# Kernel optimization log

Measured on AMD Instinct MI355X. Metric: run time of the kernel, lower is better.

The kernel has to match this reference:

```python
import jax, jax.numpy as jnp
import numpy as np

HEADS = 8
DIM_HEAD = 64
DOWN = 2

def setup_inputs() -> dict:
    key = jax.random.key(0)
    ks = jax.random.split(key, 6)
    shp = (1, 128, 16, 32, 32)
    inner = HEADS * DIM_HEAD  # 512
    return {
        "x": jax.random.normal(ks[0], shp, dtype=jnp.float32),
        "context": jax.random.normal(ks[1], shp, dtype=jnp.float32),
        "Wq": jax.random.normal(ks[2], (inner, 128), dtype=jnp.float32) * 0.02,
        "Wk": jax.random.normal(ks[3], (inner, 128), dtype=jnp.float32) * 0.02,
        "Wv": jax.random.normal(ks[4], (inner, 128), dtype=jnp.float32) * 0.02,
        "Wo": jax.random.normal(ks[5], (128, inner), dtype=jnp.float32) * 0.02,
    }

def _avg_pool3d(c, f):
    b, ch, d, h, w = c.shape
    return c.reshape(b, ch, d // f, f, h // f, f, w // f, f).mean(axis=(3, 5, 7))

def reference(x, context, Wq, Wk, Wv, Wo):
    b, c, d1, h1, w1 = x.shape
    n = d1 * h1 * w1
    scale = DIM_HEAD ** -0.5
    xf = x.reshape(b, c, n)  # [b, c, N]
    # 1x1x1 conv == channel matmul
    q = jnp.einsum('oc,bcn->bon', Wq, xf).reshape(b, HEADS, DIM_HEAD, n)
    q = jnp.swapaxes(q, -2, -1)  # [b, h, N, dh]
    ctx = _avg_pool3d(context, DOWN)
    _, _, d2, h2, w2 = ctx.shape
    m = d2 * h2 * w2
    cf = ctx.reshape(b, c, m)
    k = jnp.einsum('oc,bcm->bom', Wk, cf).reshape(b, HEADS, DIM_HEAD, m)  # [b,h,dh,M]
    v = jnp.einsum('oc,bcm->bom', Wv, cf).reshape(b, HEADS, DIM_HEAD, m)
    v = jnp.swapaxes(v, -2, -1)  # [b, h, M, dh]
    scores = jnp.einsum('bhnd,bhdm->bhnm', q, k) * scale  # [b,h,N,M]
    attn = jax.nn.softmax(scores, axis=-1)
    out = jnp.einsum('bhnm,bhmd->bhnd', attn, v)  # [b,h,N,dh]
    out = jnp.swapaxes(out, -2, -1).reshape(b, HEADS * DIM_HEAD, n)  # [b,inner,N]
    y = jnp.einsum('oc,bcn->bon', Wo, out)
    return y.reshape(b, -1, d1, h1, w1)
```

## Files before the change

### kernel.cpp

```cpp
#include <hip/hip_runtime.h>

#define N_TOK 16384
#define M_TOK 2048
#define NHEADS 8
#define DH 64
#define CIN 128
#define INNER 512

typedef __attribute__((ext_vector_type(8))) short bf16x8;
typedef __attribute__((ext_vector_type(16))) float f32x16;
typedef __attribute__((ext_vector_type(4))) unsigned int u32x4;
typedef __attribute__((ext_vector_type(2))) unsigned int u32x2;

__device__ __forceinline__ unsigned short f2bf(float f) {
    unsigned u = __float_as_uint(f);
    u += 0x7fff + ((u >> 16) & 1);
    return (unsigned short)(u >> 16);
}

__device__ __forceinline__ unsigned cvtpk(float lo, float hi) {
    unsigned r;
    asm("v_cvt_pk_bf16_f32 %0, %1, %2" : "=v"(r) : "v"(lo), "v"(hi));
    return r;
}

__device__ __forceinline__ bf16x8 mk_bf16x8(unsigned a, unsigned b, unsigned c, unsigned d) {
    union { u32x4 w; bf16x8 h; } u;
    u.w = (u32x4){a, b, c, d};
    return u.h;
}

__device__ __forceinline__ void gload16(const void* g, void* l) {
    __builtin_amdgcn_global_load_lds(
        (const __attribute__((address_space(1))) unsigned int*)g,
        (__attribute__((address_space(3))) unsigned int*)l, 16, 0, 0);
}

__global__ __launch_bounds__(256) void prep_k(const float* __restrict__ Wq,
                                              const float* __restrict__ Wo,
                                              const float* __restrict__ cin,
                                              unsigned short* __restrict__ Wqb,
                                              unsigned short* __restrict__ Wob,
                                              float* __restrict__ cout) {
    if (blockIdx.x < 64) {
        int i = (blockIdx.x * 256 + threadIdx.x) * 8;
        const float* src; unsigned short* dst; float sc;
        if (i < 65536) { src = Wq + i; dst = Wqb + i; sc = 0.125f; }
        else           { src = Wo + (i - 65536); dst = Wob + (i - 65536); sc = 1.0f; }
        float4 a = *reinterpret_cast<const float4*>(src);
        float4 b = *reinterpret_cast<const float4*>(src + 4);
        unsigned short u[8] = { f2bf(a.x * sc), f2bf(a.y * sc), f2bf(a.z * sc), f2bf(a.w * sc),
                                f2bf(b.x * sc), f2bf(b.y * sc), f2bf(b.z * sc), f2bf(b.w * sc) };
        *reinterpret_cast<uint4*>(dst) = *reinterpret_cast<uint4*>(u);
    } else {
        int idx = (blockIdx.x - 64) * 256 + threadIdx.x;
        int c = idx >> 11, m = idx & 2047;
        int d2 = m >> 8, h2 = (m >> 4) & 15, w2 = m & 15;
        const float* b = cin + c * 16384 + d2 * 2048 + h2 * 64 + w2 * 2;
        float s = b[0] + b[1] + b[32] + b[33] + b[1024] + b[1025] + b[1056] + b[1057];
        cout[idx] = s * 0.125f;
    }
}

__global__ __launch_bounds__(256) void xT_k(const float* __restrict__ x,
                                            unsigned short* __restrict__ xb) {
    __shared__ unsigned short tile[64 * 132];
    const int t = threadIdx.x;
    const int n0 = blockIdx.x * 128;
    const int cb = blockIdx.y * 64;
#pragma unroll
    for (int cc2 = 0; cc2 < 2; ++cc2)
#pragma unroll
        for (int lp = 0; lp < 4; ++lp) {
            int id = lp * 256 + t;
            int row = id >> 5, ch = id & 31;
            float4 v = *reinterpret_cast<const float4*>(
                &x[(size_t)(cb + cc2 * 32 + row) * N_TOK + n0 + ch * 4]);
            unsigned short u[4] = { f2bf(v.x), f2bf(v.y), f2bf(v.z), f2bf(v.w) };
            *reinterpret_cast<uint2*>(&tile[(cc2 * 32 + row) * 132 + ch * 4]) =
                *reinterpret_cast<uint2*>(u);
        }
    __syncthreads();
#pragma unroll
    for (int lp = 0; lp < 4; ++lp) {
        int id = lp * 256 + t;
        int n = id >> 3, cg = id & 7;
        unsigned short u[8];
#pragma unroll
        for (int j = 0; j < 8; ++j) u[j] = tile[(cg * 8 + j) * 132 + n];
        *reinterpret_cast<uint4*>(&xb[(size_t)(n0 + n) * 128 + cb + cg * 8]) =
            *reinterpret_cast<uint4*>(u);
    }
}

__global__ __launch_bounds__(256) void kvproj_k(const float* __restrict__ ctx,
                                                const float* __restrict__ Wk,
                                                const float* __restrict__ Wv,
                                                unsigned short* __restrict__ Kb,
                                                unsigned short* __restrict__ Vb) {
    const int m0 = (blockIdx.x * 256 + threadIdx.x) * 2;
    const int o0 = blockIdx.y * 8;
    const float* W = blockIdx.z ? Wv : Wk;
    float acc[8][2];
#pragma unroll
    for (int j = 0; j < 8; ++j) { acc[j][0] = 0.f; acc[j][1] = 0.f; }
    for (int c4 = 0; c4 < CIN / 4; ++c4) {
        float xa[4][2];
#pragma unroll
        for (int cc = 0; cc < 4; ++cc)
            *reinterpret_cast<float2*>(xa[cc]) =
                *reinterpret_cast<const float2*>(&ctx[(size_t)(c4 * 4 + cc) * M_TOK + m0]);
#pragma unroll
        for (int j = 0; j < 8; ++j) {
            float4 wv = *reinterpret_cast<const float4*>(&W[(o0 + j) * CIN + c4 * 4]);
#pragma unroll
            for (int k = 0; k < 2; ++k) {
                acc[j][k] = fmaf(wv.x, xa[0][k], acc[j][k]);
                acc[j][k] = fmaf(wv.y, xa[1][k], acc[j][k]);
                acc[j][k] = fmaf(wv.z, xa[2][k], acc[j][k]);
                acc[j][k] = fmaf(wv.w, xa[3][k], acc[j][k]);
            }
        }
    }
    if (blockIdx.z) {
#pragma unroll
        for (int j = 0; j < 8; ++j) {
            unsigned w0 = (unsigned)f2bf(acc[j][0]) | ((unsigned)f2bf(acc[j][1]) << 16);
            *reinterpret_cast<unsigned*>(&Vb[(size_t)(o0 + j) * M_TOK + m0]) = w0;
        }
    } else {
        const int h = o0 >> 6, d0 = o0 & 63;
#pragma unroll
        for (int k = 0; k < 2; ++k) {
            unsigned short u[8];
#pragma unroll
            for (int j = 0; j < 8; ++j) u[j] = f2bf(acc[j][k]);
            *reinterpret_cast<uint4*>(&Kb[((size_t)h * M_TOK + m0 + k) * DH + d0]) =
                *reinterpret_cast<uint4*>(u);
        }
    }
}

__global__ __launch_bounds__(256) void qproj_k(const unsigned short* __restrict__ Wqb,
                                               const unsigned short* __restrict__ xb,
                                               unsigned short* __restrict__ Qb) {
    const int t = threadIdx.x;
    const int w = t >> 6, l = t & 63;
    const int la = l & 31, lg = l >> 5;
    const int n = blockIdx.x * 32 + la;

    bf16x8 bx[8];
#pragma unroll
    for (int ks = 0; ks < 8; ++ks)
        bx[ks] = *reinterpret_cast<const bf16x8*>(xb + (size_t)n * 128 + ks * 16 + lg * 8);

    f32x16 acc[4];
#pragma unroll
    for (int os = 0; os < 4; ++os) acc[os] = (f32x16){0,0,0,0,0,0,0,0,0,0,0,0,0,0,0,0};

#pragma unroll
    for (int os = 0; os < 4; ++os) {
        const int row = w * 128 + os * 32 + la;
#pragma unroll
        for (int ks = 0; ks < 8; ++ks) {
            bf16x8 aw = *reinterpret_cast<const bf16x8*>(Wqb + (size_t)row * 128 + ks * 16 + lg * 8);
            acc[os] = __builtin_amdgcn_mfma_f32_32x32x16_bf16(aw, bx[ks], acc[os], 0, 0, 0);
        }
    }
#pragma unroll
    for (int os = 0; os < 4; ++os) {
        const int h = w * 2 + (os >> 1);
        const int dbase = (os & 1) * 32 + 4 * lg;
#pragma unroll
        for (int rr = 0; rr < 4; ++rr) {
            unsigned p0 = cvtpk(acc[os][rr * 4 + 0], acc[os][rr * 4 + 1]);
            unsigned p1 = cvtpk(acc[os][rr * 4 + 2], acc[os][rr * 4 + 3]);
            uint2 pv = make_uint2(p0, p1);
            *reinterpret_cast<uint2*>(&Qb[((size_t)h * N_TOK + n) * DH + dbase + rr * 8]) = pv;
        }
    }
}

__global__ __launch_bounds__(512, 4) void attn_k(const unsigned short* __restrict__ Qb,
                                                 const unsigned short* __restrict__ Kb,
                                                 const unsigned short* __restrict__ Vb,
                                                 unsigned short* __restrict__ Ob) {
    __shared__ __align__(16) char smem[65536];
    __shared__ float rsinv[256];

    const int t = threadIdx.x;
    const int w = t >> 6, l = t & 63;
    const int la = l & 31, lg = l >> 5;
    const int bid = blockIdx.x;
    const int h = bid & 7;
    const int n0 = (bid >> 3) * 256;

    bf16x8 aq[4];
    {
        const unsigned short* qrow = Qb + ((size_t)h * N_TOK + n0 + w * 32 + la) * DH + lg * 8;
#pragma unroll
        for (int ks = 0; ks < 4; ++ks)
            aq[ks] = *reinterpret_cast<const bf16x8*>(qrow + ks * 16);
    }

    const char* gK = (const char*)Kb + (size_t)h * M_TOK * 128;
    const char* gV = (const char*)Vb + (size_t)h * DH * 4096;

    auto stage = [&](int b, int tile) {
        char* buf = smem + b * 32768;
#pragma unroll
        for (int i = 0; i < 2; ++i) {
            int c = t + i * 512;
            int row = c >> 3, o16 = (c & 7) << 4;
            gload16(gK + (size_t)(tile * 128 + row) * 128 + (o16 ^ ((row & 7) << 4)),
                    buf + c * 16);
            int vrow = c >> 4, vo16 = (c & 15) << 4;
            gload16(gV + (size_t)vrow * 4096 + tile * 256 + (vo16 ^ ((vrow & 7) << 4)),
                    buf + 16384 + c * 16);
        }
    };

    f32x16 oacc0 = {0,0,0,0,0,0,0,0,0,0,0,0,0,0,0,0};
    f32x16 oacc1 = {0,0,0,0,0,0,0,0,0,0,0,0,0,0,0,0};
    float rs = 0.f;

    stage(0, 0);
    __syncthreads();

#pragma unroll 2
    for (int mt = 0; mt < M_TOK / 128; ++mt) {
        const int cb = (mt & 1) * 32768;
        if (mt < M_TOK / 128 - 1) stage((mt & 1) ^ 1, mt + 1);

#pragma unroll
        for (int ms = 0; ms < 4; ++ms) {
            f32x16 sacc = {0,0,0,0,0,0,0,0,0,0,0,0,0,0,0,0};
            __builtin_amdgcn_s_setprio(1);
#pragma unroll
            for (int ks = 0; ks < 4; ++ks) {
                const int row = ms * 32 + la;
                bf16x8 ak = *reinterpret_cast<const bf16x8*>(
                    smem + cb + row * 128 + ((32 * ks + 16 * lg) ^ ((row & 7) << 4)));
                sacc = __builtin_amdgcn_mfma_f32_32x32x16_bf16(ak, aq[ks], sacc, 0, 0, 0);
            }
            __builtin_amdgcn_s_setprio(0);
            float p[16];
#pragma unroll
            for (int r = 0; r < 16; ++r) { p[r] = __expf(sacc[r]); rs += p[r]; }
            u32x2 s0 = __builtin_amdgcn_permlane32_swap(cvtpk(p[0], p[1]),  cvtpk(p[4], p[5]),  false, false);
            u32x2 s1 = __builtin_amdgcn_permlane32_swap(cvtpk(p[2], p[3]),  cvtpk(p[6], p[7]),  false, false);
            u32x2 s2 = __builtin_amdgcn_permlane32_swap(cvtpk(p[8], p[9]),  cvtpk(p[12], p[13]), false, false);
            u32x2 s3 = __builtin_amdgcn_permlane32_swap(cvtpk(p[10], p[11]), cvtpk(p[14], p[15]), false, false);
            bf16x8 pa0 = mk_bf16x8(s0.x, s1.x, s0.y, s1.y);
            bf16x8 pa1 = mk_bf16x8(s2.x, s3.x, s2.y, s3.y);
            __builtin_amdgcn_s_setprio(1);
            {
                const int vrow = la, vs = (vrow & 7) << 4;
                const char* vb = smem + cb + 16384 + vrow * 256;
                bf16x8 bv0 = *reinterpret_cast<const bf16x8*>(vb + ((64 * ms + 16 * lg) ^ vs));
                bf16x8 bv1 = *reinterpret_cast<const bf16x8*>(vb + ((64 * ms + 32 + 16 * lg) ^ vs));
                oacc0 = __builtin_amdgcn_mfma_f32_32x32x16_bf16(pa0, bv0, oacc0, 0, 0, 0);
                oacc0 = __builtin_amdgcn_mfma_f32_32x32x16_bf16(pa1, bv1, oacc0, 0, 0, 0);
            }
            {
                const int vrow = 32 + la, vs = (vrow & 7) << 4;
                const char* vb = smem + cb + 16384 + vrow * 256;
                bf16x8 bv0 = *reinterpret_cast<const bf16x8*>(vb + ((64 * ms + 16 * lg) ^ vs));
                bf16x8 bv1 = *reinterpret_cast<const bf16x8*>(vb + ((64 * ms + 32 + 16 * lg) ^ vs));
                oacc1 = __builtin_amdgcn_mfma_f32_32x32x16_bf16(pa0, bv0, oacc1, 0, 0, 0);
                oacc1 = __builtin_amdgcn_mfma_f32_32x32x16_bf16(pa1, bv1, oacc1, 0, 0, 0);
            }
            __builtin_amdgcn_s_setprio(0);
        }
        __syncthreads();
    }

    rs += __shfl_xor(rs, 32);
    if (lg == 0) rsinv[w * 32 + la] = 1.0f / rs;

    float* Ot = reinterpret_cast<float*>(smem);
#pragma unroll
    for (int pass = 0; pass < 2; ++pass) {
        __syncthreads();
        if ((w >> 2) == pass) {
            const int wl = w & 3;
#pragma unroll
            for (int dt = 0; dt < 2; ++dt)
#pragma unroll
                for (int r = 0; r < 16; r += 2) {
                    int d = dt * 32 + la;
                    int n = wl * 32 + (r & 3) + 8 * (r >> 2) + 4 * lg;
                    float2 v;
                    v.x = dt ? oacc1[r] : oacc0[r];
                    v.y = dt ? oacc1[r + 1] : oacc0[r + 1];
                    *reinterpret_cast<float2*>(&Ot[d * 132 + n]) = v;
                }
        }
        __syncthreads();
#pragma unroll
        for (int i = 0; i < 2; ++i) {
            int id = i * 512 + t;
            int n = id & 127, dg = id >> 7;
            float rv = rsinv[pass * 128 + n];
            unsigned q[4];
#pragma unroll
            for (int jj = 0; jj < 4; ++jj) {
                float a = Ot[(dg * 8 + jj * 2) * 132 + n] * rv;
                float b = Ot[(dg * 8 + jj * 2 + 1) * 132 + n] * rv;
                q[jj] = cvtpk(a, b);
            }
            *reinterpret_cast<uint4*>(&Ob[(size_t)(n0 + pass * 128 + n) * INNER + h * 64 + dg * 8]) =
                *reinterpret_cast<uint4*>(q);
        }
    }
}

__global__ __launch_bounds__(256) void yproj_k(const unsigned short* __restrict__ Wob,
                                               const unsigned short* __restrict__ Ob,
                                               float* __restrict__ y) {
    const int t = threadIdx.x;
    const int w = t >> 6, l = t & 63;
    const int la = l & 31, lg = l >> 5;
    const int n = blockIdx.x * 32 + la;
    const int row = w * 32 + la;

    f32x16 acc = {0,0,0,0,0,0,0,0,0,0,0,0,0,0,0,0};
#pragma unroll 8
    for (int ks = 0; ks < 32; ++ks) {
        bf16x8 bo = *reinterpret_cast<const bf16x8*>(Ob + (size_t)n * INNER + ks * 16 + lg * 8);
        bf16x8 aw = *reinterpret_cast<const bf16x8*>(Wob + (size_t)row * INNER + ks * 16 + lg * 8);
        acc = __builtin_amdgcn_mfma_f32_32x32x16_bf16(aw, bo, acc, 0, 0, 0);
    }
#pragma unroll
    for (int rr = 0; rr < 4; ++rr)
#pragma unroll
        for (int q = 0; q < 4; ++q) {
            int o = w * 32 + 4 * lg + rr * 8 + q;
            y[(size_t)o * N_TOK + n] = acc[rr * 4 + q];
        }
}

extern "C" void kernel_launch(void* const* d_in, const int* in_sizes, int n_in,
                              void* d_out, int out_size, void* d_ws, size_t ws_size,
                              hipStream_t stream) {
    const float* x   = (const float*)d_in[0];
    const float* ctx = (const float*)d_in[1];
    const float* Wq  = (const float*)d_in[2];
    const float* Wk  = (const float*)d_in[3];
    const float* Wv  = (const float*)d_in[4];
    const float* Wo  = (const float*)d_in[5];
    float* y = (float*)d_out;

    char* W = (char*)d_ws;
    float* ctxp         = (float*)(W);
    unsigned short* Kb  = (unsigned short*)(W + 1u  * (1 << 20));
    unsigned short* Vb  = (unsigned short*)(W + 3u  * (1 << 20));
    unsigned short* xb  = (unsigned short*)(W + 5u  * (1 << 20));
    unsigned short* Wqb = (unsigned short*)(W + 9u  * (1 << 20));
    unsigned short* Wob = (unsigned short*)(W + 9u  * (1 << 20) + (256 << 10));
    unsigned short* Qb  = (unsigned short*)(W + 10u * (1 << 20));
    unsigned short* Ob  = (unsigned short*)(W + 26u * (1 << 20));

    prep_k<<<dim3(64 + (CIN * M_TOK) / 256), 256, 0, stream>>>(Wq, Wo, ctx, Wqb, Wob, ctxp);
    xT_k<<<dim3(N_TOK / 128, 2), 256, 0, stream>>>(x, xb);
    kvproj_k<<<dim3(M_TOK / 512, INNER / 8, 2), 256, 0, stream>>>(ctxp, Wk, Wv, Kb, Vb);
    qproj_k<<<dim3(N_TOK / 32), 256, 0, stream>>>(Wqb, xb, Qb);
    attn_k<<<dim3(N_TOK / 256 * NHEADS), 512, 0, stream>>>(Qb, Kb, Vb, Ob);
    yproj_k<<<dim3(N_TOK / 32), 256, 0, stream>>>(Wob, Ob, y);
}
```

Measured before the change: 139.6 us.

## Fuse x transpose into prep kernel, use exp2 softmax, simplify attention staging

Merges the x-transpose kernel into the prep kernel as extra blocks, removing one launch. Folds log2(e) into the Q weight scale so the softmax can use exp2f instead of __expf. Precomputes swizzled K/V global pointers for the async LDS staging and advances them incrementally, cutting address arithmetic in the attention loop. Halves the per-thread output count in the K/V projection to launch more blocks, at the cost of reloading context inputs more often.

Measured after the change: 194.2 us. 39.1% more time.

```diff
diff --git a/kernel.cpp b/kernel.cpp
--- a/kernel.cpp
+++ b/kernel.cpp
@@ -12,6 +12,8 @@
 typedef __attribute__((ext_vector_type(4))) unsigned int u32x4;
 typedef __attribute__((ext_vector_type(2))) unsigned int u32x2;
 
+#define QSCALE 0.18033688011112042f
+
 __device__ __forceinline__ unsigned short f2bf(float f) {
     unsigned u = __float_as_uint(f);
     u += 0x7fff + ((u >> 16) & 1);
@@ -39,57 +41,57 @@
 __global__ __launch_bounds__(256) void prep_k(const float* __restrict__ Wq,
                                               const float* __restrict__ Wo,
                                               const float* __restrict__ cin,
+                                              const float* __restrict__ x,
                                               unsigned short* __restrict__ Wqb,
                                               unsigned short* __restrict__ Wob,
-                                              float* __restrict__ cout) {
+                                              float* __restrict__ cout,
+                                              unsigned short* __restrict__ xb) {
+    __shared__ unsigned short tile[64 * 132];
+    const int t = threadIdx.x;
     if (blockIdx.x < 64) {
-        int i = (blockIdx.x * 256 + threadIdx.x) * 8;
+        int i = (blockIdx.x * 256 + t) * 8;
         const float* src; unsigned short* dst; float sc;
-        if (i < 65536) { src = Wq + i; dst = Wqb + i; sc = 0.125f; }
+        if (i < 65536) { src = Wq + i; dst = Wqb + i; sc = QSCALE; }
         else           { src = Wo + (i - 65536); dst = Wob + (i - 65536); sc = 1.0f; }
         float4 a = *reinterpret_cast<const float4*>(src);
         float4 b = *reinterpret_cast<const float4*>(src + 4);
         unsigned short u[8] = { f2bf(a.x * sc), f2bf(a.y * sc), f2bf(a.z * sc), f2bf(a.w * sc),
                                 f2bf(b.x * sc), f2bf(b.y * sc), f2bf(b.z * sc), f2bf(b.w * sc) };
         *reinterpret_cast<uint4*>(dst) = *reinterpret_cast<uint4*>(u);
-    } else {
-        int idx = (blockIdx.x - 64) * 256 + threadIdx.x;
+    } else if (blockIdx.x < 1088) {
+        int idx = (blockIdx.x - 64) * 256 + t;
         int c = idx >> 11, m = idx & 2047;
         int d2 = m >> 8, h2 = (m >> 4) & 15, w2 = m & 15;
         const float* b = cin + c * 16384 + d2 * 2048 + h2 * 64 + w2 * 2;
         float s = b[0] + b[1] + b[32] + b[33] + b[1024] + b[1025] + b[1056] + b[1057];
         cout[idx] = s * 0.125f;
-    }
-}
-
-__global__ __launch_bounds__(256) void xT_k(const float* __restrict__ x,
-                                            unsigned short* __restrict__ xb) {
-    __shared__ unsigned short tile[64 * 132];
-    const int t = threadIdx.x;
-    const int n0 = blockIdx.x * 128;
-    const int cb = blockIdx.y * 64;
-#pragma unroll
-    for (int cc2 = 0; cc2 < 2; ++cc2)
+    } else {
+        const int xbid = blockIdx.x - 1088;
+        const int n0 = (xbid & 127) * 128;
+        const int cb = (xbid >> 7) * 64;
+#pragma unroll
+        for (int cc2 = 0; cc2 < 2; ++cc2)
+#pragma unroll
+            for (int lp = 0; lp < 4; ++lp) {
+                int id = lp * 256 + t;
+                int row = id >> 5, ch = id & 31;
+                float4 v = *reinterpret_cast<const float4*>(
+                    &x[(size_t)(cb + cc2 * 32 + row) * N_TOK + n0 + ch * 4]);
+                unsigned short u[4] = { f2bf(v.x), f2bf(v.y), f2bf(v.z), f2bf(v.w) };
+                *reinterpret_cast<uint2*>(&tile[(cc2 * 32 + row) * 132 + ch * 4]) =
+                    *reinterpret_cast<uint2*>(u);
+            }
+        __syncthreads();
 #pragma unroll
         for (int lp = 0; lp < 4; ++lp) {
             int id = lp * 256 + t;
-            int row = id >> 5, ch = id & 31;
-            float4 v = *reinterpret_cast<const float4*>(
-                &x[(size_t)(cb + cc2 * 32 + row) * N_TOK + n0 + ch * 4]);
-            unsigned short u[4] = { f2bf(v.x), f2bf(v.y), f2bf(v.z), f2bf(v.w) };
-            *reinterpret_cast<uint2*>(&tile[(cc2 * 32 + row) * 132 + ch * 4]) =
-                *reinterpret_cast<uint2*>(u);
-        }
-    __syncthreads();
-#pragma unroll
-    for (int lp = 0; lp < 4; ++lp) {
-        int id = lp * 256 + t;
-        int n = id >> 3, cg = id & 7;
-        unsigned short u[8];
-#pragma unroll
-        for (int j = 0; j < 8; ++j) u[j] = tile[(cg * 8 + j) * 132 + n];
-        *reinterpret_cast<uint4*>(&xb[(size_t)(n0 + n) * 128 + cb + cg * 8]) =
-            *reinterpret_cast<uint4*>(u);
+            int n = id >> 3, cg = id & 7;
+            unsigned short u[8];
+#pragma unroll
+            for (int j = 0; j < 8; ++j) u[j] = tile[(cg * 8 + j) * 132 + n];
+            *reinterpret_cast<uint4*>(&xb[(size_t)(n0 + n) * 128 + cb + cg * 8]) =
+                *reinterpret_cast<uint4*>(u);
+        }
     }
 }
 
@@ -99,11 +101,11 @@
                                                 unsigned short* __restrict__ Kb,
                                                 unsigned short* __restrict__ Vb) {
     const int m0 = (blockIdx.x * 256 + threadIdx.x) * 2;
-    const int o0 = blockIdx.y * 8;
+    const int o0 = blockIdx.y * 4;
     const float* W = blockIdx.z ? Wv : Wk;
-    float acc[8][2];
-#pragma unroll
-    for (int j = 0; j < 8; ++j) { acc[j][0] = 0.f; acc[j][1] = 0.f; }
+    float acc[4][2];
+#pragma unroll
+    for (int j = 0; j < 4; ++j) { acc[j][0] = 0.f; acc[j][1] = 0.f; }
     for (int c4 = 0; c4 < CIN / 4; ++c4) {
         float xa[4][2];
 #pragma unroll
@@ -111,7 +113,7 @@
             *reinterpret_cast<float2*>(xa[cc]) =
                 *reinterpret_cast<const float2*>(&ctx[(size_t)(c4 * 4 + cc) * M_TOK + m0]);
 #pragma unroll
-        for (int j = 0; j < 8; ++j) {
+        for (int j = 0; j < 4; ++j) {
             float4 wv = *reinterpret_cast<const float4*>(&W[(o0 + j) * CIN + c4 * 4]);
 #pragma unroll
             for (int k = 0; k < 2; ++k) {
@@ -124,7 +126,7 @@
     }
     if (blockIdx.z) {
 #pragma unroll
-        for (int j = 0; j < 8; ++j) {
+        for (int j = 0; j < 4; ++j) {
             unsigned w0 = (unsigned)f2bf(acc[j][0]) | ((unsigned)f2bf(acc[j][1]) << 16);
             *reinterpret_cast<unsigned*>(&Vb[(size_t)(o0 + j) * M_TOK + m0]) = w0;
         }
@@ -132,11 +134,11 @@
         const int h = o0 >> 6, d0 = o0 & 63;
 #pragma unroll
         for (int k = 0; k < 2; ++k) {
-            unsigned short u[8];
-#pragma unroll
-            for (int j = 0; j < 8; ++j) u[j] = f2bf(acc[j][k]);
-            *reinterpret_cast<uint4*>(&Kb[((size_t)h * M_TOK + m0 + k) * DH + d0]) =
-                *reinterpret_cast<uint4*>(u);
+            unsigned short u[4];
+#pragma unroll
+            for (int j = 0; j < 4; ++j) u[j] = f2bf(acc[j][k]);
+            *reinterpret_cast<uint2*>(&Kb[((size_t)h * M_TOK + m0 + k) * DH + d0]) =
+                *reinterpret_cast<uint2*>(u);
         }
     }
 }
@@ -205,32 +207,33 @@
 
     const char* gK = (const char*)Kb + (size_t)h * M_TOK * 128;
     const char* gV = (const char*)Vb + (size_t)h * DH * 4096;
-
-    auto stage = [&](int b, int tile) {
+    const int r0 = t >> 3, o16 = (t & 7) << 4;
+    const int vr0 = t >> 4, vo16 = (t & 15) << 4;
+    const char* pK0 = gK + r0 * 128 + (o16 ^ ((r0 & 7) << 4));
+    const char* pK1 = pK0 + 8192;
+    const char* pV0 = gV + (size_t)vr0 * 4096 + (vo16 ^ ((vr0 & 7) << 4));
+    const char* pV1 = pV0 + 131072;
+
+    auto stageN = [&](int b) {
         char* buf = smem + b * 32768;
-#pragma unroll
-        for (int i = 0; i < 2; ++i) {
-            int c = t + i * 512;
-            int row = c >> 3, o16 = (c & 7) << 4;
-            gload16(gK + (size_t)(tile * 128 + row) * 128 + (o16 ^ ((row & 7) << 4)),
-                    buf + c * 16);
-            int vrow = c >> 4, vo16 = (c & 15) << 4;
-            gload16(gV + (size_t)vrow * 4096 + tile * 256 + (vo16 ^ ((vrow & 7) << 4)),
-                    buf + 16384 + c * 16);
-        }
+        gload16(pK0, buf + t * 16);
+        gload16(pK1, buf + t * 16 + 8192);
+        gload16(pV0, buf + 16384 + t * 16);
+        gload16(pV1, buf + 16384 + t * 16 + 8192);
+        pK0 += 16384; pK1 += 16384; pV0 += 256; pV1 += 256;
     };
 
     f32x16 oacc0 = {0,0,0,0,0,0,0,0,0,0,0,0,0,0,0,0};
     f32x16 oacc1 = {0,0,0,0,0,0,0,0,0,0,0,0,0,0,0,0};
     float rs = 0.f;
 
-    stage(0, 0);
+    stageN(0);
     __syncthreads();
 
 #pragma unroll 2
     for (int mt = 0; mt < M_TOK / 128; ++mt) {
         const int cb = (mt & 1) * 32768;
-        if (mt < M_TOK / 128 - 1) stage((mt & 1) ^ 1, mt + 1);
+        if (mt < M_TOK / 128 - 1) stageN((mt & 1) ^ 1);
 
 #pragma unroll
         for (int ms = 0; ms < 4; ++ms) {
@@ -246,7 +249,7 @@
             __builtin_amdgcn_s_setprio(0);
             float p[16];
 #pragma unroll
-            for (int r = 0; r < 16; ++r) { p[r] = __expf(sacc[r]); rs += p[r]; }
+            for (int r = 0; r < 16; ++r) { p[r] = exp2f(sacc[r]); rs += p[r]; }
             u32x2 s0 = __builtin_amdgcn_permlane32_swap(cvtpk(p[0], p[1]),  cvtpk(p[4], p[5]),  false, false);
             u32x2 s1 = __builtin_amdgcn_permlane32_swap(cvtpk(p[2], p[3]),  cvtpk(p[6], p[7]),  false, false);
             u32x2 s2 = __builtin_amdgcn_permlane32_swap(cvtpk(p[8], p[9]),  cvtpk(p[12], p[13]), false, false);
@@ -361,9 +364,8 @@
     unsigned short* Qb  = (unsigned short*)(W + 10u * (1 << 20));
     unsigned short* Ob  = (unsigned short*)(W + 26u * (1 << 20));
 
-    prep_k<<<dim3(64 + (CIN * M_TOK) / 256), 256, 0, stream>>>(Wq, Wo, ctx, Wqb, Wob, ctxp);
-    xT_k<<<dim3(N_TOK / 128, 2), 256, 0, stream>>>(x, xb);
-    kvproj_k<<<dim3(M_TOK / 512, INNER / 8, 2), 256, 0, stream>>>(ctxp, Wk, Wv, Kb, Vb);
+    prep_k<<<dim3(64 + 1024 + 256), 256, 0, stream>>>(Wq, Wo, ctx, x, Wqb, Wob, ctxp, xb);
+    kvproj_k<<<dim3(M_TOK / 512, INNER / 4, 2), 256, 0, stream>>>(ctxp, Wk, Wv, Kb, Vb);
     qproj_k<<<dim3(N_TOK / 32), 256, 0, stream>>>(Wqb, xb, Qb);
     attn_k<<<dim3(N_TOK / 256 * NHEADS), 512, 0, stream>>>(Qb, Kb, Vb, Ob);
     yproj_k<<<dim3(N_TOK / 32), 256, 0, stream>>>(Wob, Ob, y);
```
